# Kernel tuning notes

Hardware: AMD Instinct MI355X
Metric: run time of the kernel (lower is better)

Reference implementation:

```python
import jax, jax.numpy as jnp
import numpy as np

G = 7          # num_grid
SG = 12        # size_grid = 84 // 7
A = 18         # predicted_action_space
B = 8192


def _patches(x):
    # x: [B,1,84,84] -> [B, G*G, SG*SG], patch order (i rows, j cols) matching slice_grid loop
    b = x.shape[0]
    x = x.reshape(b, G, SG, G, SG)
    return x.transpose(0, 1, 3, 2, 4).reshape(b, G * G, SG * SG)


def setup_inputs() -> dict:
    key = jax.random.key(0)
    ks = jax.random.split(key, 10)
    last_states = jax.random.uniform(ks[0], (B, 1, 84, 84), jnp.float32) * 255.0
    now_states = jax.random.uniform(ks[1], (B, 1, 84, 84), jnp.float32) * 255.0
    def w(k, shape):
        return jax.random.normal(k, shape, jnp.float32) * 0.05
    return {
        "last_states": last_states,
        "now_states": now_states,
        # mlp_e: 288 -> 256 -> 128 -> 18
        "We1": w(ks[2], (2 * SG * SG, 256)), "be1": jnp.zeros((256,), jnp.float32),
        "We2": w(ks[3], (256, 128)),          "be2": jnp.zeros((128,), jnp.float32),
        "We3": w(ks[4], (128, A)),            "be3": jnp.zeros((A,), jnp.float32),
        # mlp_alpha: 144 -> 64 -> 64 -> 1
        "Wa1": w(ks[5], (SG * SG, 64)), "ba1": jnp.zeros((64,), jnp.float32),
        "Wa2": w(ks[6], (64, 64)),       "ba2": jnp.zeros((64,), jnp.float32),
        "Wa3": w(ks[7], (64, 1)),        "ba3": jnp.zeros((1,), jnp.float32),
    }


def reference(last_states, now_states, We1, be1, We2, be2, We3, be3,
              Wa1, ba1, Wa2, ba2, Wa3, ba3):
    last = last_states / 255.0
    now = now_states / 255.0
    p_now = _patches(now)            # [B, P, 144]
    p_last = _patches(last)          # [B, P, 144]

    # alpha: per-patch scalar via small MLP, softmax over patches
    h = jax.nn.relu(jnp.einsum('bpf,fo->bpo', p_now, Wa1) + ba1)
    h = jax.nn.relu(jnp.einsum('bpf,fo->bpo', h, Wa2) + ba2)
    alpha_logits = (jnp.einsum('bpf,fo->bpo', h, Wa3) + ba3)[..., 0]   # [B, P]
    alpha = jax.nn.softmax(alpha_logits, axis=1)

    # e: per-patch action logits from [diff, now]
    e_in = jnp.concatenate([p_now - p_last, p_now], axis=-1)           # [B, P, 288]
    g = jax.nn.relu(jnp.einsum('bpf,fo->bpo', e_in, We1) + be1)
    g = jax.nn.relu(jnp.einsum('bpf,fo->bpo', g, We2) + be2)
    e = jnp.einsum('bpf,fo->bpo', g, We3) + be3                        # [B, P, A]

    predicted_action_log_probs = jax.nn.log_softmax(
        (e * alpha[..., None]).sum(axis=1), axis=1)                    # [B, A]
    predicted_action_log_probs_each = jax.nn.log_softmax(e, axis=2)    # [B, P, A]
    loss_ent = (alpha * jnp.log(alpha)).sum(axis=1).mean()
    return predicted_action_log_probs, loss_ent, predicted_action_log_probs_each
```

## Files before the change

kernel.cpp:

```cpp
#include <hip/hip_runtime.h>
#include <math.h>

#define NPCH 49
#define NA 18
#define NB 8192
#define TOTAL (NB*NPCH)

typedef __attribute__((ext_vector_type(8))) short bf16x8;
typedef __attribute__((ext_vector_type(4))) float f32x4;

__device__ __forceinline__ unsigned short f2bf(float f) {
    unsigned int u = __float_as_uint(f);
    return (unsigned short)((u + 0x7FFFu + ((u >> 16) & 1u)) >> 16);
}

#define MF(a,b,c) __builtin_amdgcn_mfma_f32_16x16x32_bf16((a),(b),(c),0,0,0)
#define RAWBAR() do { \
    asm volatile("s_waitcnt lgkmcnt(0)" ::: "memory"); \
    __builtin_amdgcn_s_barrier(); \
    asm volatile("" ::: "memory"); \
} while (0)

#define WS_US (256*512)

__global__ __launch_bounds__(256)
void prep_weights(const float* __restrict__ We1, const float* __restrict__ We2,
                  const float* __restrict__ We3, const float* __restrict__ Wa1,
                  const float* __restrict__ Wa2, unsigned short* __restrict__ wst)
{
    int i = blockIdx.x * 256 + threadIdx.x;
    if (i >= WS_US) return;
    const int fs = i >> 9, l = (i >> 3) & 63, j = i & 7;
    const int kh = ((l >> 4) << 3) + j;
    const int nl = l & 15;
    float v = 0.0f;
    if (fs < 20) {
        int s = fs >> 2, w = fs & 3;
        int k = s * 32 + kh, n = w * 16 + nl;
        v = (k < 144) ? Wa1[k * 64 + n] : 0.0f;
    } else if (fs < 28) {
        int q = fs - 20, s = q >> 2, w = q & 3;
        v = Wa2[(s * 32 + kh) * 64 + (w * 16 + nl)];
    } else if (fs < 32) {
        v = 0.0f;
    } else if (fs < 176) {
        int q = fs - 32, s = q >> 4, nt = (q >> 2) & 3, w = q & 3;
        v = We1[(s * 32 + kh) * 256 + (w * 64 + nt * 16 + nl)];
    } else if (fs < 240) {
        int q = fs - 176, s = q >> 3, nt = (q >> 2) & 1, w = q & 3;
        v = We2[(s * 32 + kh) * 128 + (w * 32 + nt * 16 + nl)];
    } else if (fs < 248) {
        int q = fs - 240, s = q >> 1, nt = q & 1;
        int n = nt * 16 + nl;
        v = (n < NA) ? We3[(s * 32 + kh) * NA + n] : 0.0f;
    }
    wst[i] = f2bf(v);
}

__global__ __launch_bounds__(256, 3)
void fused_mfma_kernel(const float* __restrict__ last_s, const float* __restrict__ now_s,
                       const unsigned short* __restrict__ wstream,
                       const float* __restrict__ be1, const float* __restrict__ be2,
                       const float* __restrict__ be3, const float* __restrict__ ba1,
                       const float* __restrict__ ba2, const float* __restrict__ ba3,
                       const float* __restrict__ Wa3,
                       float* __restrict__ out_each, float* __restrict__ ws_alpha)
{
    __shared__ __align__(16) unsigned char smem[46080];
    unsigned short* Ein = (unsigned short*)smem;
    unsigned short* H1  = (unsigned short*)smem;
    unsigned short* H2  = (unsigned short*)smem;
    unsigned short* HA1 = (unsigned short*)(smem + 36864);
    float*          APT = (float*)(smem + 45056);

    const int t    = threadIdx.x;
    const int lane = t & 63;
    const int wid  = t >> 6;
    const int g    = lane >> 4;
    const int rl   = lane & 15;
    const int img  = blockIdx.x;

#define GFRAG(fs) (*(const bf16x8*)(wstream + (size_t)(fs) * 512 + lane * 8))

    bf16x8 wa1f[5], wa2f[2];
    #pragma unroll
    for (int s = 0; s < 5; ++s) wa1f[s] = GFRAG(s * 4 + wid);
    #pragma unroll
    for (int s = 0; s < 2; ++s) wa2f[s] = GFRAG(20 + s * 4 + wid);
    bf16x8 wA[4], wB[4], wC[4];
    #pragma unroll
    for (int nt = 0; nt < 4; ++nt) wA[nt] = GFRAG(32 + 0 * 16 + nt * 4 + wid);
    #pragma unroll
    for (int nt = 0; nt < 4; ++nt) wB[nt] = GFRAG(32 + 1 * 16 + nt * 4 + wid);
    #pragma unroll
    for (int nt = 0; nt < 4; ++nt) wC[nt] = GFRAG(32 + 2 * 16 + nt * 4 + wid);

    {
        const float* nowI  = now_s  + (size_t)img * 7056;
        const float* lastI = last_s + (size_t)img * 7056;
        #pragma unroll
        for (int it = 0; it < 7; ++it) {
            const int i = t + it * 256;
            if (i < 1764) {
                const float4 n4 = *(const float4*)(nowI + i * 4);
                const float4 l4 = *(const float4*)(lastI + i * 4);
                const int px = i * 4, row = px / 84, col = px - row * 84;
                const int pi = row / 12, fr = row - pi * 12;
                const int pj = col / 12, fc = col - pj * 12;
                const int p = pi * 7 + pj, f = fr * 12 + fc;
                const int wp = p >> 4, rp = p & 15;
                const float k255 = 1.0f / 255.0f;
                ushort4 d4, w4;
                d4.x = f2bf((n4.x - l4.x) * k255); d4.y = f2bf((n4.y - l4.y) * k255);
                d4.z = f2bf((n4.z - l4.z) * k255); d4.w = f2bf((n4.w - l4.w) * k255);
                w4.x = f2bf(n4.x * k255); w4.y = f2bf(n4.y * k255);
                w4.z = f2bf(n4.z * k255); w4.w = f2bf(n4.w * k255);
                const int s1 = f >> 5, g1 = (f >> 3) & 3, j1 = f & 7;
                *(ushort4*)(Ein + (wp * 9 + s1) * 512 + g1 * 128 + rp * 8 + j1) = d4;
                const int k2 = 144 + f;
                const int s2 = k2 >> 5, g2 = (k2 >> 3) & 3, j2 = k2 & 7;
                *(ushort4*)(Ein + (wp * 9 + s2) * 512 + g2 * 128 + rp * 8 + j2) = w4;
            }
        }
    }
    RAWBAR();

    const int colA = wid * 16 + rl;
    f32x4 accA[4];
    {
        const float b1 = ba1[colA];
        #pragma unroll
        for (int mt = 0; mt < 4; ++mt) accA[mt] = (f32x4){b1, b1, b1, b1};
        #pragma unroll
        for (int sa = 0; sa < 5; ++sa) {
            int ok = 144 + sa * 32 + g * 8;
            if (ok > 280) ok = 280;
            #pragma unroll
            for (int mt = 0; mt < 4; ++mt) {
                const bf16x8 af = *(const bf16x8*)(Ein + (mt * 9 + (ok >> 5)) * 512 +
                                                   ((ok >> 3) & 3) * 128 + rl * 8);
                accA[mt] = MF(af, wa1f[sa], accA[mt]);
            }
        }
        const int sA  = wid >> 1;
        const int hiA = (wid & 1) * 2 + (rl >> 3);
        const int jA  = rl & 7;
        #pragma unroll
        for (int mt = 0; mt < 4; ++mt) {
            unsigned short* base = HA1 + (mt * 2 + sA) * 512 + hiA * 128 + g * 32 + jA;
            #pragma unroll
            for (int r = 0; r < 4; ++r)
                base[r * 8] = f2bf(fmaxf(accA[mt][r], 0.0f));
        }
    }
    RAWBAR();

    {
        const float b2 = ba2[colA];
        const float w3 = Wa3[colA];
        f32x4 accB[4];
        #pragma unroll
        for (int mt = 0; mt < 4; ++mt) accB[mt] = (f32x4){b2, b2, b2, b2};
        #pragma unroll
        for (int s = 0; s < 2; ++s) {
            #pragma unroll
            for (int mt = 0; mt < 4; ++mt) {
                const bf16x8 af = *(const bf16x8*)(HA1 + (mt * 2 + s) * 512 + lane * 8);
                accB[mt] = MF(af, wa2f[s], accB[mt]);
            }
        }
        #pragma unroll
        for (int mt = 0; mt < 4; ++mt) {
            #pragma unroll
            for (int r = 0; r < 4; ++r) {
                float v = fmaxf(accB[mt][r], 0.0f) * w3;
                v += __shfl_xor(v, 1); v += __shfl_xor(v, 2);
                v += __shfl_xor(v, 4); v += __shfl_xor(v, 8);
                if (rl == 0) APT[wid * 64 + mt * 16 + g * 4 + r] = v;
            }
        }
    }
    RAWBAR();
    if (t < NPCH)
        ws_alpha[img * NPCH + t] = APT[t] + APT[64 + t] + APT[128 + t] + APT[192 + t] + ba3[0];

    f32x4 acc1[4][4];
    #pragma unroll
    for (int nt = 0; nt < 4; ++nt) {
        const float b = be1[wid * 64 + nt * 16 + rl];
        #pragma unroll
        for (int mt = 0; mt < 4; ++mt) acc1[mt][nt] = (f32x4){b, b, b, b};
    }

#define E1_STEP(W, s, sn) do { \
    const bf16x8 x0_ = *(const bf16x8*)(Ein + (0 * 9 + (s)) * 512 + lane * 8); \
    const bf16x8 x1_ = *(const bf16x8*)(Ein + (1 * 9 + (s)) * 512 + lane * 8); \
    const bf16x8 x2_ = *(const bf16x8*)(Ein + (2 * 9 + (s)) * 512 + lane * 8); \
    const bf16x8 x3_ = *(const bf16x8*)(Ein + (3 * 9 + (s)) * 512 + lane * 8); \
    _Pragma("unroll") \
    for (int nt = 0; nt < 4; ++nt) { \
        acc1[0][nt] = MF(x0_, W[nt], acc1[0][nt]); \
        acc1[1][nt] = MF(x1_, W[nt], acc1[1][nt]); \
        acc1[2][nt] = MF(x2_, W[nt], acc1[2][nt]); \
        acc1[3][nt] = MF(x3_, W[nt], acc1[3][nt]); \
    } \
    if ((sn) <= 8) { \
        _Pragma("unroll") \
        for (int nt = 0; nt < 4; ++nt) W[nt] = GFRAG(32 + (sn) * 16 + nt * 4 + wid); \
    } \
} while (0)

    E1_STEP(wA, 0, 3); E1_STEP(wB, 1, 4); E1_STEP(wC, 2, 5);
    E1_STEP(wA, 3, 6); E1_STEP(wB, 4, 7); E1_STEP(wC, 5, 8);
    E1_STEP(wA, 6, 9); E1_STEP(wB, 7, 9); E1_STEP(wC, 8, 9);
#undef E1_STEP

    RAWBAR();

    #pragma unroll
    for (int mt = 0; mt < 4; ++mt) {
        #pragma unroll
        for (int nt = 0; nt < 4; ++nt) {
            const int col = wid * 64 + nt * 16 + rl;
            unsigned short* base = H1 + (mt * 8 + (col >> 5)) * 512 +
                                   ((col >> 3) & 3) * 128 + g * 32 + (col & 7);
            #pragma unroll
            for (int r = 0; r < 4; ++r)
                base[r * 8] = f2bf(fmaxf(acc1[mt][nt][r], 0.0f));
        }
    }
    RAWBAR();

    f32x4 acc2[4][2];
    #pragma unroll
    for (int nt = 0; nt < 2; ++nt) {
        const float b = be2[wid * 32 + nt * 16 + rl];
        #pragma unroll
        for (int mt = 0; mt < 4; ++mt) acc2[mt][nt] = (f32x4){b, b, b, b};
    }
    bf16x8 vA[2], vB[2], vC[2];
    #pragma unroll
    for (int nt = 0; nt < 2; ++nt) vA[nt] = GFRAG(176 + 0 * 8 + nt * 4 + wid);
    #pragma unroll
    for (int nt = 0; nt < 2; ++nt) vB[nt] = GFRAG(176 + 1 * 8 + nt * 4 + wid);
    #pragma unroll
    for (int nt = 0; nt < 2; ++nt) vC[nt] = GFRAG(176 + 2 * 8 + nt * 4 + wid);

#define E2_STEP(V, s2, sn) do { \
    const bf16x8 x0_ = *(const bf16x8*)(H1 + (0 * 8 + (s2)) * 512 + lane * 8); \
    const bf16x8 x1_ = *(const bf16x8*)(H1 + (1 * 8 + (s2)) * 512 + lane * 8); \
    const bf16x8 x2_ = *(const bf16x8*)(H1 + (2 * 8 + (s2)) * 512 + lane * 8); \
    const bf16x8 x3_ = *(const bf16x8*)(H1 + (3 * 8 + (s2)) * 512 + lane * 8); \
    _Pragma("unroll") \
    for (int nt = 0; nt < 2; ++nt) { \
        acc2[0][nt] = MF(x0_, V[nt], acc2[0][nt]); \
        acc2[1][nt] = MF(x1_, V[nt], acc2[1][nt]); \
        acc2[2][nt] = MF(x2_, V[nt], acc2[2][nt]); \
        acc2[3][nt] = MF(x3_, V[nt], acc2[3][nt]); \
    } \
    if ((sn) <= 7) { \
        _Pragma("unroll") \
        for (int nt = 0; nt < 2; ++nt) V[nt] = GFRAG(176 + (sn) * 8 + nt * 4 + wid); \
    } \
} while (0)

    E2_STEP(vA, 0, 3); E2_STEP(vB, 1, 4); E2_STEP(vC, 2, 5);
    E2_STEP(vA, 3, 6); E2_STEP(vB, 4, 7); E2_STEP(vC, 5, 8);
    E2_STEP(vA, 6, 8); E2_STEP(vB, 7, 8);
#undef E2_STEP

    bf16x8 w3f[8];
    #pragma unroll
    for (int q = 0; q < 8; ++q) w3f[q] = GFRAG(240 + q);

    RAWBAR();

    #pragma unroll
    for (int mt = 0; mt < 4; ++mt) {
        #pragma unroll
        for (int nt = 0; nt < 2; ++nt) {
            const int c2 = nt * 16 + rl;
            unsigned short* base = H2 + (mt * 4 + wid) * 512 +
                                   ((c2 >> 3) & 3) * 128 + g * 32 + (c2 & 7);
            #pragma unroll
            for (int r = 0; r < 4; ++r)
                base[r * 8] = f2bf(fmaxf(acc2[mt][nt][r], 0.0f));
        }
    }
    RAWBAR();

    {
        f32x4 acc3[2];
        #pragma unroll
        for (int nt = 0; nt < 2; ++nt) {
            const int col = nt * 16 + rl;
            const float b = (col < NA) ? be3[col] : 0.0f;
            acc3[nt] = (f32x4){b, b, b, b};
        }
        #pragma unroll
        for (int s = 0; s < 4; ++s) {
            const bf16x8 af = *(const bf16x8*)(H2 + (wid * 4 + s) * 512 + lane * 8);
            acc3[0] = MF(af, w3f[s * 2 + 0], acc3[0]);
            acc3[1] = MF(af, w3f[s * 2 + 1], acc3[1]);
        }
        const bool v1 = (rl < 2);
        #pragma unroll
        for (int r = 0; r < 4; ++r) {
            const int p3 = wid * 16 + g * 4 + r;
            float x0 = acc3[0][r];
            float x1 = acc3[1][r];
            float m = fmaxf(x0, v1 ? x1 : -3.0e38f);
            m = fmaxf(m, __shfl_xor(m, 1)); m = fmaxf(m, __shfl_xor(m, 2));
            m = fmaxf(m, __shfl_xor(m, 4)); m = fmaxf(m, __shfl_xor(m, 8));
            float sm = expf(x0 - m) + (v1 ? expf(x1 - m) : 0.0f);
            sm += __shfl_xor(sm, 1); sm += __shfl_xor(sm, 2);
            sm += __shfl_xor(sm, 4); sm += __shfl_xor(sm, 8);
            const float L = m + logf(sm);
            if (p3 < NPCH) {
                float* o = out_each + (size_t)(img * NPCH + p3) * NA;
                o[rl] = x0 - L;
                if (v1) o[16 + rl] = x1 - L;
            }
        }
    }
#undef GFRAG
}

__global__ __launch_bounds__(64)
void alpha_combine_kernel(const float* __restrict__ ws_alpha,
                          const float* __restrict__ out_each,
                          float* __restrict__ out_probs,
                          float* __restrict__ ws_ent)
{
    const int b = blockIdx.x;
    const int lane = threadIdx.x;

    float lg = (lane < NPCH) ? ws_alpha[b * NPCH + lane] : -3.0e38f;
    float m = lg;
    #pragma unroll
    for (int off = 32; off > 0; off >>= 1) m = fmaxf(m, __shfl_xor(m, off, 64));
    float ex = (lane < NPCH) ? expf(lg - m) : 0.0f;
    float s = ex;
    #pragma unroll
    for (int off = 32; off > 0; off >>= 1) s += __shfl_xor(s, off, 64);
    const float ls = logf(s);
    const float alpha = ex / s;

    float ent = (lane < NPCH) ? alpha * (lg - m - ls) : 0.0f;
    #pragma unroll
    for (int off = 32; off > 0; off >>= 1) ent += __shfl_xor(ent, off, 64);
    if (lane == 0) ws_ent[b] = ent;

    float acc = 0.0f;
    const float* eb = out_each + (size_t)b * NPCH * NA;
    for (int p = 0; p < NPCH; ++p) {
        const float ap = __shfl(alpha, p, 64);
        if (lane < NA) acc += ap * eb[p * NA + lane];
    }
    float mm = (lane < NA) ? acc : -3.0e38f;
    #pragma unroll
    for (int off = 32; off > 0; off >>= 1) mm = fmaxf(mm, __shfl_xor(mm, off, 64));
    float ee = (lane < NA) ? expf(acc - mm) : 0.0f;
    #pragma unroll
    for (int off = 32; off > 0; off >>= 1) ee += __shfl_xor(ee, off, 64);
    if (lane < NA) out_probs[b * NA + lane] = acc - mm - logf(ee);
}

__global__ __launch_bounds__(256)
void ent_reduce_kernel(const float* __restrict__ ws_ent, float* __restrict__ out_scalar)
{
    float s = 0.0f;
    for (int i = threadIdx.x; i < NB; i += 256) s += ws_ent[i];
    #pragma unroll
    for (int off = 32; off > 0; off >>= 1) s += __shfl_xor(s, off, 64);
    __shared__ float ps[4];
    if ((threadIdx.x & 63) == 0) ps[threadIdx.x >> 6] = s;
    __syncthreads();
    if (threadIdx.x == 0)
        out_scalar[0] = (ps[0] + ps[1] + ps[2] + ps[3]) * (1.0f / NB);
}

extern "C" void kernel_launch(void* const* d_in, const int* in_sizes, int n_in,
                              void* d_out, int out_size, void* d_ws, size_t ws_size,
                              hipStream_t stream)
{
    (void)in_sizes; (void)n_in; (void)out_size; (void)ws_size;

    const float* last_s = (const float*)d_in[0];
    const float* now_s  = (const float*)d_in[1];
    const float* We1 = (const float*)d_in[2];  const float* be1 = (const float*)d_in[3];
    const float* We2 = (const float*)d_in[4];  const float* be2 = (const float*)d_in[5];
    const float* We3 = (const float*)d_in[6];  const float* be3 = (const float*)d_in[7];
    const float* Wa1 = (const float*)d_in[8];  const float* ba1 = (const float*)d_in[9];
    const float* Wa2 = (const float*)d_in[10]; const float* ba2 = (const float*)d_in[11];
    const float* Wa3 = (const float*)d_in[12]; const float* ba3 = (const float*)d_in[13];

    float* out = (float*)d_out;
    float* out_probs = out;
    float* out_ent   = out + NB * NA;
    float* out_each  = out + NB * NA + 1;

    float* ws_alpha = (float*)d_ws;
    float* ws_ent   = ws_alpha + TOTAL;
    unsigned short* wst = (unsigned short*)(ws_ent + NB);

    prep_weights<<<dim3((WS_US + 255) / 256), dim3(256), 0, stream>>>(
        We1, We2, We3, Wa1, Wa2, wst);

    fused_mfma_kernel<<<dim3(NB), dim3(256), 0, stream>>>(
        last_s, now_s, wst, be1, be2, be3, ba1, ba2, ba3, Wa3,
        out_each, ws_alpha);

    alpha_combine_kernel<<<dim3(NB), dim3(64), 0, stream>>>(
        ws_alpha, out_each, out_probs, ws_ent);

    ent_reduce_kernel<<<dim3(1), dim3(256), 0, stream>>>(ws_ent, out_ent);
}
```

Measured before the change: 253.2 us.

## Fuse alpha layer-1 into e layer-1 GEMM and fold combine kernel into main kernel

Packs the Wa1 weights as a fifth N-tile next to We1 so the alpha first layer shares the A-fragment loads and MFMA pass with the e first layer. It also drops the separate alpha_combine kernel: alpha softmax, entropy and the weighted log-softmax now run in wave 0 at the end of the main kernel, reading e values from shared memory. This removes a launch and the global round-trip of out_each and alpha. Float-to-bf16 rounding now uses packed hardware convert instructions. The costs are more accumulator registers (a 4x5 tile), which may hurt occupancy, and a serial tail on a single wave.

```diff
diff --git a/kernel.cpp b/kernel.cpp
--- a/kernel.cpp
+++ b/kernel.cpp
@@ -21,7 +21,7 @@
     asm volatile("" ::: "memory"); \
 } while (0)
 
-#define WS_US (256*512)
+#define WS_US (260*512)
 
 __global__ __launch_bounds__(256)
 void prep_weights(const float* __restrict__ We1, const float* __restrict__ We2,
@@ -34,27 +34,37 @@
     const int kh = ((l >> 4) << 3) + j;
     const int nl = l & 15;
     float v = 0.0f;
-    if (fs < 20) {
-        int s = fs >> 2, w = fs & 3;
-        int k = s * 32 + kh, n = w * 16 + nl;
-        v = (k < 144) ? Wa1[k * 64 + n] : 0.0f;
-    } else if (fs < 28) {
-        int q = fs - 20, s = q >> 2, w = q & 3;
+    if (fs < 180) {
+        int s = fs / 20, rem = fs - s * 20;
+        int w = rem / 5, nt = rem - w * 5;
+        int k = s * 32 + kh;
+        if (nt < 4) v = We1[k * 256 + (w * 64 + nt * 16 + nl)];
+        else        v = (k >= 144) ? Wa1[(k - 144) * 64 + (w * 16 + nl)] : 0.0f;
+    } else if (fs < 188) {
+        int q = fs - 180, s = q >> 2, w = q & 3;
         v = Wa2[(s * 32 + kh) * 64 + (w * 16 + nl)];
-    } else if (fs < 32) {
-        v = 0.0f;
-    } else if (fs < 176) {
-        int q = fs - 32, s = q >> 4, nt = (q >> 2) & 3, w = q & 3;
-        v = We1[(s * 32 + kh) * 256 + (w * 64 + nt * 16 + nl)];
-    } else if (fs < 240) {
-        int q = fs - 176, s = q >> 3, nt = (q >> 2) & 1, w = q & 3;
+    } else if (fs < 252) {
+        int q = fs - 188, s = q >> 3, rem = q & 7, w = rem >> 1, nt = rem & 1;
         v = We2[(s * 32 + kh) * 128 + (w * 32 + nt * 16 + nl)];
-    } else if (fs < 248) {
-        int q = fs - 240, s = q >> 1, nt = q & 1;
+    } else {
+        int q = fs - 252, s = q >> 1, nt = q & 1;
         int n = nt * 16 + nl;
         v = (n < NA) ? We3[(s * 32 + kh) * NA + n] : 0.0f;
     }
     wst[i] = f2bf(v);
+}
+
+__device__ __forceinline__ void wb_frag(unsigned short* base, f32x4 a)
+{
+    float r0 = fmaxf(a[0], 0.f), r1 = fmaxf(a[1], 0.f);
+    float r2 = fmaxf(a[2], 0.f), r3 = fmaxf(a[3], 0.f);
+    unsigned u01, u23;
+    asm("v_cvt_pk_bf16_f32 %0, %1, %2" : "=v"(u01) : "v"(r0), "v"(r1));
+    asm("v_cvt_pk_bf16_f32 %0, %1, %2" : "=v"(u23) : "v"(r2), "v"(r3));
+    base[0]  = (unsigned short)u01;
+    base[8]  = (unsigned short)(u01 >> 16);
+    base[16] = (unsigned short)u23;
+    base[24] = (unsigned short)(u23 >> 16);
 }
 
 __global__ __launch_bounds__(256, 3)
@@ -64,7 +74,8 @@
                        const float* __restrict__ be3, const float* __restrict__ ba1,
                        const float* __restrict__ ba2, const float* __restrict__ ba3,
                        const float* __restrict__ Wa3,
-                       float* __restrict__ out_each, float* __restrict__ ws_alpha)
+                       float* __restrict__ out_each, float* __restrict__ out_probs,
+                       float* __restrict__ ws_ent)
 {
     __shared__ __align__(16) unsigned char smem[46080];
     unsigned short* Ein = (unsigned short*)smem;
@@ -72,6 +83,8 @@
     unsigned short* H2  = (unsigned short*)smem;
     unsigned short* HA1 = (unsigned short*)(smem + 36864);
     float*          APT = (float*)(smem + 45056);
+    float*          ALG = (float*)(smem + 36864);
+    float*          OE  = (float*)(smem + 37120);
 
     const int t    = threadIdx.x;
     const int lane = t & 63;
@@ -82,18 +95,16 @@
 
 #define GFRAG(fs) (*(const bf16x8*)(wstream + (size_t)(fs) * 512 + lane * 8))
 
-    bf16x8 wa1f[5], wa2f[2];
-    #pragma unroll
-    for (int s = 0; s < 5; ++s) wa1f[s] = GFRAG(s * 4 + wid);
-    #pragma unroll
-    for (int s = 0; s < 2; ++s) wa2f[s] = GFRAG(20 + s * 4 + wid);
-    bf16x8 wA[4], wB[4], wC[4];
-    #pragma unroll
-    for (int nt = 0; nt < 4; ++nt) wA[nt] = GFRAG(32 + 0 * 16 + nt * 4 + wid);
-    #pragma unroll
-    for (int nt = 0; nt < 4; ++nt) wB[nt] = GFRAG(32 + 1 * 16 + nt * 4 + wid);
-    #pragma unroll
-    for (int nt = 0; nt < 4; ++nt) wC[nt] = GFRAG(32 + 2 * 16 + nt * 4 + wid);
+    bf16x8 wa2f[2];
+    #pragma unroll
+    for (int s = 0; s < 2; ++s) wa2f[s] = GFRAG(180 + s * 4 + wid);
+    bf16x8 wA[5], wB[5], wC[5];
+    #pragma unroll
+    for (int nt = 0; nt < 5; ++nt) wA[nt] = GFRAG( 0 + wid * 5 + nt);
+    #pragma unroll
+    for (int nt = 0; nt < 5; ++nt) wB[nt] = GFRAG(20 + wid * 5 + nt);
+    #pragma unroll
+    for (int nt = 0; nt < 5; ++nt) wC[nt] = GFRAG(40 + wid * 5 + nt);
 
     {
         const float* nowI  = now_s  + (size_t)img * 7056;
@@ -110,51 +121,91 @@
                 const int p = pi * 7 + pj, f = fr * 12 + fc;
                 const int wp = p >> 4, rp = p & 15;
                 const float k255 = 1.0f / 255.0f;
-                ushort4 d4, w4;
-                d4.x = f2bf((n4.x - l4.x) * k255); d4.y = f2bf((n4.y - l4.y) * k255);
-                d4.z = f2bf((n4.z - l4.z) * k255); d4.w = f2bf((n4.w - l4.w) * k255);
-                w4.x = f2bf(n4.x * k255); w4.y = f2bf(n4.y * k255);
-                w4.z = f2bf(n4.z * k255); w4.w = f2bf(n4.w * k255);
+                float d0 = (n4.x - l4.x) * k255, d1 = (n4.y - l4.y) * k255;
+                float d2 = (n4.z - l4.z) * k255, d3 = (n4.w - l4.w) * k255;
+                float w0 = n4.x * k255, w1 = n4.y * k255;
+                float w2 = n4.z * k255, w3 = n4.w * k255;
+                unsigned da, db, wa, wb;
+                asm("v_cvt_pk_bf16_f32 %0, %1, %2" : "=v"(da) : "v"(d0), "v"(d1));
+                asm("v_cvt_pk_bf16_f32 %0, %1, %2" : "=v"(db) : "v"(d2), "v"(d3));
+                asm("v_cvt_pk_bf16_f32 %0, %1, %2" : "=v"(wa) : "v"(w0), "v"(w1));
+                asm("v_cvt_pk_bf16_f32 %0, %1, %2" : "=v"(wb) : "v"(w2), "v"(w3));
                 const int s1 = f >> 5, g1 = (f >> 3) & 3, j1 = f & 7;
-                *(ushort4*)(Ein + (wp * 9 + s1) * 512 + g1 * 128 + rp * 8 + j1) = d4;
+                *(uint2*)(Ein + (wp * 9 + s1) * 512 + g1 * 128 + rp * 8 + j1) = (uint2){da, db};
                 const int k2 = 144 + f;
                 const int s2 = k2 >> 5, g2 = (k2 >> 3) & 3, j2 = k2 & 7;
-                *(ushort4*)(Ein + (wp * 9 + s2) * 512 + g2 * 128 + rp * 8 + j2) = w4;
+                *(uint2*)(Ein + (wp * 9 + s2) * 512 + g2 * 128 + rp * 8 + j2) = (uint2){wa, wb};
             }
         }
     }
     RAWBAR();
 
-    const int colA = wid * 16 + rl;
-    f32x4 accA[4];
+    f32x4 acc1[4][5];
+    #pragma unroll
+    for (int nt = 0; nt < 4; ++nt) {
+        const float b = be1[wid * 64 + nt * 16 + rl];
+        #pragma unroll
+        for (int mt = 0; mt < 4; ++mt) acc1[mt][nt] = (f32x4){b, b, b, b};
+    }
     {
-        const float b1 = ba1[colA];
-        #pragma unroll
-        for (int mt = 0; mt < 4; ++mt) accA[mt] = (f32x4){b1, b1, b1, b1};
-        #pragma unroll
-        for (int sa = 0; sa < 5; ++sa) {
-            int ok = 144 + sa * 32 + g * 8;
-            if (ok > 280) ok = 280;
-            #pragma unroll
-            for (int mt = 0; mt < 4; ++mt) {
-                const bf16x8 af = *(const bf16x8*)(Ein + (mt * 9 + (ok >> 5)) * 512 +
-                                                   ((ok >> 3) & 3) * 128 + rl * 8);
-                accA[mt] = MF(af, wa1f[sa], accA[mt]);
-            }
-        }
+        const float b = ba1[wid * 16 + rl];
+        #pragma unroll
+        for (int mt = 0; mt < 4; ++mt) acc1[mt][4] = (f32x4){b, b, b, b};
+    }
+
+#define E1M_STEP(W, s, sn) do { \
+    const bf16x8 x0_ = *(const bf16x8*)(Ein + (0 * 9 + (s)) * 512 + lane * 8); \
+    const bf16x8 x1_ = *(const bf16x8*)(Ein + (1 * 9 + (s)) * 512 + lane * 8); \
+    const bf16x8 x2_ = *(const bf16x8*)(Ein + (2 * 9 + (s)) * 512 + lane * 8); \
+    const bf16x8 x3_ = *(const bf16x8*)(Ein + (3 * 9 + (s)) * 512 + lane * 8); \
+    _Pragma("unroll") \
+    for (int nt = 0; nt < 5; ++nt) { \
+        acc1[0][nt] = MF(x0_, W[nt], acc1[0][nt]); \
+        acc1[1][nt] = MF(x1_, W[nt], acc1[1][nt]); \
+        acc1[2][nt] = MF(x2_, W[nt], acc1[2][nt]); \
+        acc1[3][nt] = MF(x3_, W[nt], acc1[3][nt]); \
+    } \
+    if ((sn) <= 8) { \
+        _Pragma("unroll") \
+        for (int nt = 0; nt < 5; ++nt) W[nt] = GFRAG((sn) * 20 + wid * 5 + nt); \
+    } \
+} while (0)
+
+    E1M_STEP(wA, 0, 3); E1M_STEP(wB, 1, 4); E1M_STEP(wC, 2, 5);
+    E1M_STEP(wA, 3, 6); E1M_STEP(wB, 4, 7); E1M_STEP(wC, 5, 8);
+    E1M_STEP(wA, 6, 9); E1M_STEP(wB, 7, 9); E1M_STEP(wC, 8, 9);
+#undef E1M_STEP
+
+    bf16x8 vA[2], vB[2], vC[2];
+    #pragma unroll
+    for (int nt = 0; nt < 2; ++nt) vA[nt] = GFRAG(188 + 0 * 8 + wid * 2 + nt);
+    #pragma unroll
+    for (int nt = 0; nt < 2; ++nt) vB[nt] = GFRAG(188 + 1 * 8 + wid * 2 + nt);
+    #pragma unroll
+    for (int nt = 0; nt < 2; ++nt) vC[nt] = GFRAG(188 + 2 * 8 + wid * 2 + nt);
+
+    RAWBAR();
+
+    #pragma unroll
+    for (int mt = 0; mt < 4; ++mt) {
+        #pragma unroll
+        for (int nt = 0; nt < 4; ++nt) {
+            const int col = wid * 64 + nt * 16 + rl;
+            wb_frag(H1 + (mt * 8 + (col >> 5)) * 512 + ((col >> 3) & 3) * 128 +
+                    g * 32 + (col & 7), acc1[mt][nt]);
+        }
+    }
+    {
         const int sA  = wid >> 1;
         const int hiA = (wid & 1) * 2 + (rl >> 3);
         const int jA  = rl & 7;
         #pragma unroll
-        for (int mt = 0; mt < 4; ++mt) {
-            unsigned short* base = HA1 + (mt * 2 + sA) * 512 + hiA * 128 + g * 32 + jA;
-            #pragma unroll
-            for (int r = 0; r < 4; ++r)
-                base[r * 8] = f2bf(fmaxf(accA[mt][r], 0.0f));
-        }
-    }
-    RAWBAR();
-
+        for (int mt = 0; mt < 4; ++mt)
+            wb_frag(HA1 + (mt * 2 + sA) * 512 + hiA * 128 + g * 32 + jA, acc1[mt][4]);
+    }
+    RAWBAR();
+
+    const int colA = wid * 16 + rl;
     {
         const float b2 = ba2[colA];
         const float w3 = Wa3[colA];
@@ -180,56 +231,6 @@
             }
         }
     }
-    RAWBAR();
-    if (t < NPCH)
-        ws_alpha[img * NPCH + t] = APT[t] + APT[64 + t] + APT[128 + t] + APT[192 + t] + ba3[0];
-
-    f32x4 acc1[4][4];
-    #pragma unroll
-    for (int nt = 0; nt < 4; ++nt) {
-        const float b = be1[wid * 64 + nt * 16 + rl];
-        #pragma unroll
-        for (int mt = 0; mt < 4; ++mt) acc1[mt][nt] = (f32x4){b, b, b, b};
-    }
-
-#define E1_STEP(W, s, sn) do { \
-    const bf16x8 x0_ = *(const bf16x8*)(Ein + (0 * 9 + (s)) * 512 + lane * 8); \
-    const bf16x8 x1_ = *(const bf16x8*)(Ein + (1 * 9 + (s)) * 512 + lane * 8); \
-    const bf16x8 x2_ = *(const bf16x8*)(Ein + (2 * 9 + (s)) * 512 + lane * 8); \
-    const bf16x8 x3_ = *(const bf16x8*)(Ein + (3 * 9 + (s)) * 512 + lane * 8); \
-    _Pragma("unroll") \
-    for (int nt = 0; nt < 4; ++nt) { \
-        acc1[0][nt] = MF(x0_, W[nt], acc1[0][nt]); \
-        acc1[1][nt] = MF(x1_, W[nt], acc1[1][nt]); \
-        acc1[2][nt] = MF(x2_, W[nt], acc1[2][nt]); \
-        acc1[3][nt] = MF(x3_, W[nt], acc1[3][nt]); \
-    } \
-    if ((sn) <= 8) { \
-        _Pragma("unroll") \
-        for (int nt = 0; nt < 4; ++nt) W[nt] = GFRAG(32 + (sn) * 16 + nt * 4 + wid); \
-    } \
-} while (0)
-
-    E1_STEP(wA, 0, 3); E1_STEP(wB, 1, 4); E1_STEP(wC, 2, 5);
-    E1_STEP(wA, 3, 6); E1_STEP(wB, 4, 7); E1_STEP(wC, 5, 8);
-    E1_STEP(wA, 6, 9); E1_STEP(wB, 7, 9); E1_STEP(wC, 8, 9);
-#undef E1_STEP
-
-    RAWBAR();
-
-    #pragma unroll
-    for (int mt = 0; mt < 4; ++mt) {
-        #pragma unroll
-        for (int nt = 0; nt < 4; ++nt) {
-            const int col = wid * 64 + nt * 16 + rl;
-            unsigned short* base = H1 + (mt * 8 + (col >> 5)) * 512 +
-                                   ((col >> 3) & 3) * 128 + g * 32 + (col & 7);
-            #pragma unroll
-            for (int r = 0; r < 4; ++r)
-                base[r * 8] = f2bf(fmaxf(acc1[mt][nt][r], 0.0f));
-        }
-    }
-    RAWBAR();
 
     f32x4 acc2[4][2];
     #pragma unroll
@@ -238,14 +239,6 @@
         #pragma unroll
         for (int mt = 0; mt < 4; ++mt) acc2[mt][nt] = (f32x4){b, b, b, b};
     }
-    bf16x8 vA[2], vB[2], vC[2];
-    #pragma unroll
-    for (int nt = 0; nt < 2; ++nt) vA[nt] = GFRAG(176 + 0 * 8 + nt * 4 + wid);
-    #pragma unroll
-    for (int nt = 0; nt < 2; ++nt) vB[nt] = GFRAG(176 + 1 * 8 + nt * 4 + wid);
-    #pragma unroll
-    for (int nt = 0; nt < 2; ++nt) vC[nt] = GFRAG(176 + 2 * 8 + nt * 4 + wid);
-
 #define E2_STEP(V, s2, sn) do { \
     const bf16x8 x0_ = *(const bf16x8*)(H1 + (0 * 8 + (s2)) * 512 + lane * 8); \
     const bf16x8 x1_ = *(const bf16x8*)(H1 + (1 * 8 + (s2)) * 512 + lane * 8); \
@@ -260,7 +253,7 @@
     } \
     if ((sn) <= 7) { \
         _Pragma("unroll") \
-        for (int nt = 0; nt < 2; ++nt) V[nt] = GFRAG(176 + (sn) * 8 + nt * 4 + wid); \
+        for (int nt = 0; nt < 2; ++nt) V[nt] = GFRAG(188 + (sn) * 8 + wid * 2 + nt); \
     } \
 } while (0)
 
@@ -271,20 +264,20 @@
 
     bf16x8 w3f[8];
     #pragma unroll
-    for (int q = 0; q < 8; ++q) w3f[q] = GFRAG(240 + q);
-
-    RAWBAR();
+    for (int q = 0; q < 8; ++q) w3f[q] = GFRAG(252 + q);
+
+    RAWBAR();
+
+    if (t < NPCH)
+        ALG[t] = APT[t] + APT[64 + t] + APT[128 + t] + APT[192 + t] + ba3[0];
 
     #pragma unroll
     for (int mt = 0; mt < 4; ++mt) {
         #pragma unroll
         for (int nt = 0; nt < 2; ++nt) {
             const int c2 = nt * 16 + rl;
-            unsigned short* base = H2 + (mt * 4 + wid) * 512 +
-                                   ((c2 >> 3) & 3) * 128 + g * 32 + (c2 & 7);
-            #pragma unroll
-            for (int r = 0; r < 4; ++r)
-                base[r * 8] = f2bf(fmaxf(acc2[mt][nt][r], 0.0f));
+            wb_frag(H2 + (mt * 4 + wid) * 512 + ((c2 >> 3) & 3) * 128 +
+                    g * 32 + (c2 & 7), acc2[mt][nt]);
         }
     }
     RAWBAR();
@@ -318,52 +311,50 @@
             const float L = m + logf(sm);
             if (p3 < NPCH) {
                 float* o = out_each + (size_t)(img * NPCH + p3) * NA;
-                o[rl] = x0 - L;
-                if (v1) o[16 + rl] = x1 - L;
+                const float y0 = x0 - L;
+                o[rl] = y0;
+                OE[p3 * NA + rl] = y0;
+                if (v1) {
+                    const float y1 = x1 - L;
+                    o[16 + rl] = y1;
+                    OE[p3 * NA + 16 + rl] = y1;
+                }
             }
         }
     }
+    RAWBAR();
+
+    if (wid == 0) {
+        float lg = (lane < NPCH) ? ALG[lane] : -3.0e38f;
+        float m = lg;
+        #pragma unroll
+        for (int off = 32; off > 0; off >>= 1) m = fmaxf(m, __shfl_xor(m, off, 64));
+        float ex = (lane < NPCH) ? expf(lg - m) : 0.0f;
+        float s = ex;
+        #pragma unroll
+        for (int off = 32; off > 0; off >>= 1) s += __shfl_xor(s, off, 64);
+        const float ls = logf(s);
+        const float alpha = ex / s;
+
+        float ent = (lane < NPCH) ? alpha * (lg - m - ls) : 0.0f;
+        #pragma unroll
+        for (int off = 32; off > 0; off >>= 1) ent += __shfl_xor(ent, off, 64);
+        if (lane == 0) ws_ent[img] = ent;
+
+        float acc = 0.0f;
+        for (int p = 0; p < NPCH; ++p) {
+            const float ap = __shfl(alpha, p, 64);
+            if (lane < NA) acc += ap * OE[p * NA + lane];
+        }
+        float mm = (lane < NA) ? acc : -3.0e38f;
+        #pragma unroll
+        for (int off = 32; off > 0; off >>= 1) mm = fmaxf(mm, __shfl_xor(mm, off, 64));
+        float ee = (lane < NA) ? expf(acc - mm) : 0.0f;
+        #pragma unroll
+        for (int off = 32; off > 0; off >>= 1) ee += __shfl_xor(ee, off, 64);
+        if (lane < NA) out_probs[img * NA + lane] = acc - mm - logf(ee);
+    }
 #undef GFRAG
-}
-
-__global__ __launch_bounds__(64)
-void alpha_combine_kernel(const float* __restrict__ ws_alpha,
-                          const float* __restrict__ out_each,
-                          float* __restrict__ out_probs,
-                          float* __restrict__ ws_ent)
-{
-    const int b = blockIdx.x;
-    const int lane = threadIdx.x;
-
-    float lg = (lane < NPCH) ? ws_alpha[b * NPCH + lane] : -3.0e38f;
-    float m = lg;
-    #pragma unroll
-    for (int off = 32; off > 0; off >>= 1) m = fmaxf(m, __shfl_xor(m, off, 64));
-    float ex = (lane < NPCH) ? expf(lg - m) : 0.0f;
-    float s = ex;
-    #pragma unroll
-    for (int off = 32; off > 0; off >>= 1) s += __shfl_xor(s, off, 64);
-    const float ls = logf(s);
-    const float alpha = ex / s;
-
-    float ent = (lane < NPCH) ? alpha * (lg - m - ls) : 0.0f;
-    #pragma unroll
-    for (int off = 32; off > 0; off >>= 1) ent += __shfl_xor(ent, off, 64);
-    if (lane == 0) ws_ent[b] = ent;
-
-    float acc = 0.0f;
-    const float* eb = out_each + (size_t)b * NPCH * NA;
-    for (int p = 0; p < NPCH; ++p) {
-        const float ap = __shfl(alpha, p, 64);
-        if (lane < NA) acc += ap * eb[p * NA + lane];
-    }
-    float mm = (lane < NA) ? acc : -3.0e38f;
-    #pragma unroll
-    for (int off = 32; off > 0; off >>= 1) mm = fmaxf(mm, __shfl_xor(mm, off, 64));
-    float ee = (lane < NA) ? expf(acc - mm) : 0.0f;
-    #pragma unroll
-    for (int off = 32; off > 0; off >>= 1) ee += __shfl_xor(ee, off, 64);
-    if (lane < NA) out_probs[b * NA + lane] = acc - mm - logf(ee);
 }
 
 __global__ __launch_bounds__(256)
@@ -400,8 +391,7 @@
     float* out_ent   = out + NB * NA;
     float* out_each  = out + NB * NA + 1;
 
-    float* ws_alpha = (float*)d_ws;
-    float* ws_ent   = ws_alpha + TOTAL;
+    float* ws_ent = (float*)d_ws;
     unsigned short* wst = (unsigned short*)(ws_ent + NB);
 
     prep_weights<<<dim3((WS_US + 255) / 256), dim3(256), 0, stream>>>(
@@ -409,10 +399,7 @@
 
     fused_mfma_kernel<<<dim3(NB), dim3(256), 0, stream>>>(
         last_s, now_s, wst, be1, be2, be3, ba1, ba2, ba3, Wa3,
-        out_each, ws_alpha);
-
-    alpha_combine_kernel<<<dim3(NB), dim3(64), 0, stream>>>(
-        ws_alpha, out_each, out_probs, ws_ent);
+        out_each, out_probs, ws_ent);
 
     ent_reduce_kernel<<<dim3(1), dim3(256), 0, stream>>>(ws_ent, out_ent);
 }
```

After: 296.1 us. 16.9% more time.
